# Performance work log

Measured on AMD Instinct MI355X. Metric: run time of the kernel, lower is better.

Reference implementation:

```python
import jax, jax.numpy as jnp
import numpy as np

B, V, F, P = 16, 100000, 200000, 65536


def _sample_one(verts, faces, e1, e2, u):
    # verts: [V,3], faces: [F,3], e1/e2/u: [P]
    tris = verts[faces]                      # [F,3,3] irregular gather
    vec1 = tris[:, 1, :] - tris[:, 0, :]
    vec2 = tris[:, 2, :] - tris[:, 0, :]
    normals = jnp.cross(vec1, vec2)          # [F,3]
    areas = jnp.linalg.norm(normals, axis=1) / 2.0  # [F]
    # area-weighted categorical sampling via inverse CDF (deterministic given u)
    cdf = jnp.cumsum(areas)
    cdf = cdf / cdf[-1]
    idx = jnp.clip(jnp.searchsorted(jax.lax.stop_gradient(cdf), u), 0, F - 1)  # [P]
    sampled_tris = tris[idx]                 # [P,3,3]
    unit_normals = normals / (areas[:, None] * 2.0)
    sampled_normals = unit_normals[idx]      # [P,3]
    # barycentric weights (Osada et al.)
    s = jnp.sqrt(e1)
    w = jnp.stack([1.0 - s, (1.0 - e2) * s, e2 * s], axis=1)[:, :, None]  # [P,3,1]
    points = jnp.sum(sampled_tris * w, axis=1)  # [P,3]
    return points, sampled_normals


def setup_inputs() -> dict:
    key = jax.random.key(0)
    k1, k2, k3, k4, k5 = jax.random.split(key, 5)
    vertices_batch = jax.random.normal(k1, (B, V, 3), dtype=jnp.float32)
    faces_batch = jax.random.randint(k2, (B, F, 3), 0, V, dtype=jnp.int64)
    eps1 = jax.random.uniform(k3, (B, P), dtype=jnp.float32)
    eps2 = jax.random.uniform(k4, (B, P), dtype=jnp.float32)
    u = jax.random.uniform(k5, (B, P), dtype=jnp.float32)
    return {"vertices_batch": vertices_batch, "faces_batch": faces_batch,
            "eps1": eps1, "eps2": eps2, "u": u}


def reference(vertices_batch, faces_batch, eps1, eps2, u):
    points, normals = jax.vmap(_sample_one)(vertices_batch, faces_batch, eps1, eps2, u)
    return points, normals  # ([B,P,3], [B,P,3])
```

## Files before the change

### kernel.cpp

```cpp
#include <hip/hip_runtime.h>

#pragma clang fp contract(off)

#define NB 16
#define NV 100000
#define NF 200000
#define NP 65536

#define B16 16
#define NW0 12500
#define NW1 782
#define NW2 49
#define NW3 4

#define TREE_LVL 12
#define TREE_N   (1 << TREE_LVL)

__device__ __forceinline__ void xcd_map(int p, int& batch, int& chunk) {
    int r = p & 15;
    batch = 2 * (r & 7) + (r >> 3);
    chunk = p >> 4;
}

__device__ __forceinline__ void load_face(const int* __restrict__ faces,
                                          long long fidx,
                                          int& i0, int& i1, int& i2) {
    const int* p = faces + fidx * 3;
    i0 = p[0]; i1 = p[1]; i2 = p[2];
}

__global__ void area_prefix_kernel(const float* __restrict__ verts,
                                   const int* __restrict__ faces,
                                   float* __restrict__ cdf,
                                   float* __restrict__ s0) {
    __shared__ float S[256];
    int batch, chunk;
    xcd_map(blockIdx.x, batch, chunk);
    int tid = threadIdx.x;
    int i = chunk * 256 + tid;
    bool valid = (i < NF);
    float a = 0.0f;
    if (valid) {
        size_t gid = (size_t)batch * NF + i;
        const float* vb = verts + (size_t)batch * NV * 3;
        int i0, i1, i2;
        load_face(faces, (long long)gid, i0, i1, i2);
        float ax = vb[3 * i0 + 0], ay = vb[3 * i0 + 1], az = vb[3 * i0 + 2];
        float bx = vb[3 * i1 + 0], by = vb[3 * i1 + 1], bz = vb[3 * i1 + 2];
        float cx = vb[3 * i2 + 0], cy = vb[3 * i2 + 1], cz = vb[3 * i2 + 2];
        float v1x = bx - ax, v1y = by - ay, v1z = bz - az;
        float v2x = cx - ax, v2y = cy - ay, v2z = cz - az;
        float nx = fmaf(v1y, v2z, -(v1z * v2y));
        float ny = fmaf(v1z, v2x, -(v1x * v2z));
        float nz = fmaf(v1x, v2y, -(v1y * v2x));
        float ss = fmaf(nz, nz, fmaf(nx, nx, ny * ny));
        float nrm = sqrtf(ss);
        a = nrm / 2.0f;
    }
    S[tid] = a;
    __syncthreads();
    if (valid) {
        int base = tid & ~15;
        float run = S[base];
        for (int p = base + 1; p <= tid; ++p) run = run + S[p];
        cdf[(size_t)batch * NF + i] = run;
        if ((tid & 15) == 15)
            s0[(size_t)batch * NW0 + (i >> 4)] = run;
    }
}

__global__ void midscan16_kernel(const float* __restrict__ s0g, float* __restrict__ S0g) {
    __shared__ float t0[NW0];
    __shared__ float t1[NW1];
    __shared__ float t2[NW2];
    __shared__ float t3[NW3];
    int b = blockIdx.x;
    for (int i = threadIdx.x; i < NW0; i += blockDim.x)
        t0[i] = s0g[(size_t)b * NW0 + i];
    __syncthreads();
    for (int w = threadIdx.x; w < NW1; w += blockDim.x) {
        int st = w * B16, en = st + B16 < NW0 ? st + B16 : NW0;
        float run = 0.0f;
        for (int p = st; p < en; ++p) { run = run + t0[p]; t0[p] = run; }
        t1[w] = run;
    }
    __syncthreads();
    for (int w = threadIdx.x; w < NW2; w += blockDim.x) {
        int st = w * B16, en = st + B16 < NW1 ? st + B16 : NW1;
        float run = 0.0f;
        for (int p = st; p < en; ++p) { run = run + t1[p]; t1[p] = run; }
        t2[w] = run;
    }
    __syncthreads();
    for (int w = threadIdx.x; w < NW3; w += blockDim.x) {
        int st = w * B16, en = st + B16 < NW2 ? st + B16 : NW2;
        float run = 0.0f;
        for (int p = st; p < en; ++p) { run = run + t2[p]; t2[p] = run; }
        t3[w] = run;
    }
    __syncthreads();
    if (threadIdx.x == 0) {
        float run = 0.0f;
        for (int k = 0; k < NW3; ++k) { run = run + t3[k]; t3[k] = run; }
    }
    __syncthreads();
    for (int i = threadIdx.x; i < NW2; i += blockDim.x) {
        int w = i >> 4;
        float off = (w > 0) ? t3[w - 1] : 0.0f;
        t2[i] = off + t2[i];
    }
    __syncthreads();
    for (int i = threadIdx.x; i < NW1; i += blockDim.x) {
        int w = i >> 4;
        float off = (w > 0) ? t2[w - 1] : 0.0f;
        t1[i] = off + t1[i];
    }
    __syncthreads();
    for (int i = threadIdx.x; i < NW0; i += blockDim.x) {
        int w = i >> 4;
        float off = (w > 0) ? t1[w - 1] : 0.0f;
        t0[i] = off + t0[i];
    }
    __syncthreads();
    for (int i = threadIdx.x; i < NW0; i += blockDim.x)
        S0g[(size_t)b * NW0 + i] = t0[i];
}

__global__ void fused_norm_kernel(float* __restrict__ cdf,
                                  const float* __restrict__ s0,
                                  const float* __restrict__ S0) {
    int batch, chunk;
    xcd_map(blockIdx.x, batch, chunk);
    int i = chunk * 256 + threadIdx.x;
    if (i >= NF) return;
    const float* S0b = S0 + (size_t)batch * NW0;
    float total = S0b[NW0 - 2] + s0[(size_t)batch * NW0 + NW0 - 1];
    float rcp = 1.0f / total;
    int j = i >> 4;
    float off = (j > 0) ? S0b[j - 1] : 0.0f;
    float* p = cdf + (size_t)batch * NF + i;
    *p = (off + *p) * rcp;
}

__global__ void treebuild_kernel(const float* __restrict__ cdf, float* __restrict__ Tg) {
    int b = blockIdx.x;
    const float* c = cdf + (size_t)b * NF;
    float* T = Tg + (size_t)b * TREE_N;
    for (int n = 1 + threadIdx.x; n < TREE_N; n += blockDim.x) {
        int k = 31 - __clz(n);
        int low = 0, high = NF;
        for (int j = k - 1; j >= 0; --j) {
            int mid = (low + high) >> 1;
            if ((n >> j) & 1) low = mid; else high = mid;
        }
        T[n] = c[(low + high) >> 1];
    }
}

__global__ void sample_kernel(const float* __restrict__ verts,
                              const int* __restrict__ faces,
                              const float* __restrict__ e1,
                              const float* __restrict__ e2,
                              const float* __restrict__ u,
                              const float* __restrict__ cdf,
                              const float* __restrict__ Tg,
                              float* __restrict__ out) {
    __shared__ float T[TREE_N];
    int batch, chunk;
    xcd_map(blockIdx.x, batch, chunk);
    int b = batch;
    const float* c = cdf + (size_t)b * NF;
    const float* Tb = Tg + (size_t)b * TREE_N;

    for (int n = threadIdx.x; n < TREE_N; n += blockDim.x)
        T[n] = Tb[n];
    __syncthreads();

    int li = chunk * 256 + threadIdx.x;
    int gid = (b << 16) + li;

    float uv = u[gid];
    int low = 0, high = NF, node = 1;
    #pragma unroll
    for (int it = 0; it < TREE_LVL; ++it) {
        int mid = (low + high) >> 1;
        bool gl = (uv <= T[node]);
        node = 2 * node + (gl ? 0 : 1);
        if (gl) high = mid; else low = mid;
    }
    #pragma unroll
    for (int it = TREE_LVL; it < 18; ++it) {
        int mid = (low + high) >> 1;
        bool gl = (uv <= c[mid]);
        if (gl) high = mid; else low = mid;
    }
    int idx = high < NF - 1 ? high : NF - 1;

    const float* vb = verts + (size_t)b * NV * 3;
    int i0, i1, i2;
    load_face(faces, (long long)b * NF + idx, i0, i1, i2);
    double ax = vb[3 * i0 + 0], ay = vb[3 * i0 + 1], az = vb[3 * i0 + 2];
    double bx = vb[3 * i1 + 0], by = vb[3 * i1 + 1], bz = vb[3 * i1 + 2];
    double cx = vb[3 * i2 + 0], cy = vb[3 * i2 + 1], cz = vb[3 * i2 + 2];

    double v1x = bx - ax, v1y = by - ay, v1z = bz - az;
    double v2x = cx - ax, v2y = cy - ay, v2z = cz - az;
    double nx = v1y * v2z - v1z * v2y;
    double ny = v1z * v2x - v1x * v2z;
    double nz = v1x * v2y - v1y * v2x;
    double ss = (nx * nx + ny * ny) + nz * nz;
    double nrm = sqrt(ss);
    double unx = nx / nrm, uny = ny / nrm, unz = nz / nrm;

    double s = sqrt((double)e1[gid]);
    double t = (double)e2[gid];
    double w0 = 1.0 - s;
    double w1 = (1.0 - t) * s;
    double w2 = t * s;
    double px = (ax * w0 + bx * w1) + cx * w2;
    double py = (ay * w0 + by * w1) + cy * w2;
    double pz = (az * w0 + bz * w1) + cz * w2;

    size_t po = (size_t)gid * 3;
    out[po + 0] = (float)px;
    out[po + 1] = (float)py;
    out[po + 2] = (float)pz;
    size_t no = (size_t)NB * NP * 3 + po;
    out[no + 0] = (float)unx;
    out[no + 1] = (float)uny;
    out[no + 2] = (float)unz;
}

extern "C" void kernel_launch(void* const* d_in, const int* in_sizes, int n_in,
                              void* d_out, int out_size, void* d_ws, size_t ws_size,
                              hipStream_t stream) {
    const float* verts = (const float*)d_in[0];
    const int*   faces = (const int*)d_in[1];
    const float* e1    = (const float*)d_in[2];
    const float* e2    = (const float*)d_in[3];
    const float* u     = (const float*)d_in[4];
    float* out = (float*)d_out;

    char* ws = (char*)d_ws;
    float* cdf = (float*)(ws + 512);
    float* s0  = (float*)(ws + 512 + (size_t)NB * NF * 4);
    float* S0  = (float*)(ws + 512 + (size_t)NB * NF * 4 + (size_t)NB * NW0 * 4);
    float* Tg  = (float*)(ws + 512 + (size_t)NB * NF * 4 + 2 * (size_t)NB * NW0 * 4);

    area_prefix_kernel<<<16 * 782, 256, 0, stream>>>(verts, faces, cdf, s0);

    midscan16_kernel<<<NB, 256, 0, stream>>>(s0, S0);

    fused_norm_kernel<<<16 * 782, 256, 0, stream>>>(cdf, s0, S0);

    treebuild_kernel<<<NB, 256, 0, stream>>>(cdf, Tg);

    sample_kernel<<<16 * 256, 256, 0, stream>>>(verts, faces, e1, e2, u, cdf, Tg, out);
}
```

Baseline: 162.1 us.

## Fuse midscan and tree build, apply CDF offset lazily during search

Removes the full-array normalization pass over the CDF and folds the tree build into the midscan kernel. The tree nodes are built directly from the scanned block offsets and the reciprocal of the total. The sample kernel now applies the block offset and reciprocal on the fly for each global-memory probe in the lower search levels. This saves one full read-modify-write of 16x200k floats and two launches, at the cost of an extra dependent load per search step in the sampler.

```diff
diff --git a/kernel.cpp b/kernel.cpp
--- a/kernel.cpp
+++ b/kernel.cpp
@@ -69,7 +69,11 @@
     }
 }
 
-__global__ void midscan16_kernel(const float* __restrict__ s0g, float* __restrict__ S0g) {
+__global__ void midscan_tree_kernel(const float* __restrict__ s0g,
+                                    const float* __restrict__ cdf,
+                                    float* __restrict__ S0g,
+                                    float* __restrict__ Tg,
+                                    float* __restrict__ rcps) {
     __shared__ float t0[NW0];
     __shared__ float t1[NW1];
     __shared__ float t2[NW2];
@@ -124,26 +128,10 @@
     __syncthreads();
     for (int i = threadIdx.x; i < NW0; i += blockDim.x)
         S0g[(size_t)b * NW0 + i] = t0[i];
-}
-
-__global__ void fused_norm_kernel(float* __restrict__ cdf,
-                                  const float* __restrict__ s0,
-                                  const float* __restrict__ S0) {
-    int batch, chunk;
-    xcd_map(blockIdx.x, batch, chunk);
-    int i = chunk * 256 + threadIdx.x;
-    if (i >= NF) return;
-    const float* S0b = S0 + (size_t)batch * NW0;
-    float total = S0b[NW0 - 2] + s0[(size_t)batch * NW0 + NW0 - 1];
+
+    float total = t0[NW0 - 2] + s0g[(size_t)b * NW0 + NW0 - 1];
     float rcp = 1.0f / total;
-    int j = i >> 4;
-    float off = (j > 0) ? S0b[j - 1] : 0.0f;
-    float* p = cdf + (size_t)batch * NF + i;
-    *p = (off + *p) * rcp;
-}
-
-__global__ void treebuild_kernel(const float* __restrict__ cdf, float* __restrict__ Tg) {
-    int b = blockIdx.x;
+    if (threadIdx.x == 0) rcps[b] = rcp;
     const float* c = cdf + (size_t)b * NF;
     float* T = Tg + (size_t)b * TREE_N;
     for (int n = 1 + threadIdx.x; n < TREE_N; n += blockDim.x) {
@@ -153,7 +141,10 @@
             int mid = (low + high) >> 1;
             if ((n >> j) & 1) low = mid; else high = mid;
         }
-        T[n] = c[(low + high) >> 1];
+        int m = (low + high) >> 1;
+        int w = m >> 4;
+        float off = (w > 0) ? t0[w - 1] : 0.0f;
+        T[n] = (off + c[m]) * rcp;
     }
 }
 
@@ -163,23 +154,27 @@
                               const float* __restrict__ e2,
                               const float* __restrict__ u,
                               const float* __restrict__ cdf,
+                              const float* __restrict__ S0g,
                               const float* __restrict__ Tg,
+                              const float* __restrict__ rcps,
                               float* __restrict__ out) {
     __shared__ float T[TREE_N];
     int batch, chunk;
     xcd_map(blockIdx.x, batch, chunk);
     int b = batch;
     const float* c = cdf + (size_t)b * NF;
+    const float* S0b = S0g + (size_t)b * NW0;
     const float* Tb = Tg + (size_t)b * TREE_N;
+    float rcp = rcps[b];
+
+    int li = chunk * 256 + threadIdx.x;
+    int gid = (b << 16) + li;
+    float uv = u[gid];
 
     for (int n = threadIdx.x; n < TREE_N; n += blockDim.x)
         T[n] = Tb[n];
     __syncthreads();
 
-    int li = chunk * 256 + threadIdx.x;
-    int gid = (b << 16) + li;
-
-    float uv = u[gid];
     int low = 0, high = NF, node = 1;
     #pragma unroll
     for (int it = 0; it < TREE_LVL; ++it) {
@@ -191,7 +186,10 @@
     #pragma unroll
     for (int it = TREE_LVL; it < 18; ++it) {
         int mid = (low + high) >> 1;
-        bool gl = (uv <= c[mid]);
+        int w = mid >> 4;
+        float off = (w > 0) ? S0b[w - 1] : 0.0f;
+        float val = (off + c[mid]) * rcp;
+        bool gl = (uv <= val);
         if (gl) high = mid; else low = mid;
     }
     int idx = high < NF - 1 ? high : NF - 1;
@@ -242,18 +240,17 @@
     float* out = (float*)d_out;
 
     char* ws = (char*)d_ws;
-    float* cdf = (float*)(ws + 512);
-    float* s0  = (float*)(ws + 512 + (size_t)NB * NF * 4);
-    float* S0  = (float*)(ws + 512 + (size_t)NB * NF * 4 + (size_t)NB * NW0 * 4);
-    float* Tg  = (float*)(ws + 512 + (size_t)NB * NF * 4 + 2 * (size_t)NB * NW0 * 4);
+    float* cdf  = (float*)(ws + 512);
+    float* s0   = (float*)(ws + 512 + (size_t)NB * NF * 4);
+    float* S0   = (float*)(ws + 512 + (size_t)NB * NF * 4 + (size_t)NB * NW0 * 4);
+    float* Tg   = (float*)(ws + 512 + (size_t)NB * NF * 4 + 2 * (size_t)NB * NW0 * 4);
+    float* rcps = (float*)(ws + 512 + (size_t)NB * NF * 4 + 2 * (size_t)NB * NW0 * 4
+                               + (size_t)NB * TREE_N * 4);
 
     area_prefix_kernel<<<16 * 782, 256, 0, stream>>>(verts, faces, cdf, s0);
 
-    midscan16_kernel<<<NB, 256, 0, stream>>>(s0, S0);
-
-    fused_norm_kernel<<<16 * 782, 256, 0, stream>>>(cdf, s0, S0);
-
-    treebuild_kernel<<<NB, 256, 0, stream>>>(cdf, Tg);
-
-    sample_kernel<<<16 * 256, 256, 0, stream>>>(verts, faces, e1, e2, u, cdf, Tg, out);
-}
+    midscan_tree_kernel<<<NB, 256, 0, stream>>>(s0, cdf, S0, Tg, rcps);
+
+    sample_kernel<<<16 * 256, 256, 0, stream>>>(verts, faces, e1, e2, u,
+                                                cdf, S0, Tg, rcps, out);
+}
```

Result: slower. 172.1 us (+6.2%).
